# Performance work log

Hardware: AMD Instinct MI355X
Metric: run time of the kernel (lower is better)

Reference implementation:

```python
import jax, jax.numpy as jnp
import numpy as np

HIDDEN = 1024
N_HEADS = 16
HEAD_DIM = HIDDEN // N_HEADS
WINDOW = 256
HALF_W = WINDOW // 2  # 128
GLOBAL_TOKENS = (0,)


def setup_inputs() -> dict:
    key = jax.random.key(0)
    ks = jax.random.split(key, 5)
    B, S = 1, 4096
    scale = 0.02
    return {
        "x": jax.random.normal(ks[0], (B, S, HIDDEN), dtype=jnp.float32),
        "Wq": jax.random.normal(ks[1], (HIDDEN, HIDDEN), dtype=jnp.float32) * scale,
        "Wk": jax.random.normal(ks[2], (HIDDEN, HIDDEN), dtype=jnp.float32) * scale,
        "Wv": jax.random.normal(ks[3], (HIDDEN, HIDDEN), dtype=jnp.float32) * scale,
        "Wo": jax.random.normal(ks[4], (HIDDEN, HIDDEN), dtype=jnp.float32) * scale,
    }


def _longformer_mask(seq_len: int) -> jnp.ndarray:
    # sliding window |i-j| <= half_w, plus full rows/cols for global tokens
    idx = jnp.arange(seq_len)
    mask = jnp.abs(idx[:, None] - idx[None, :]) <= HALF_W
    for g in GLOBAL_TOKENS:
        if 0 <= g < seq_len:
            mask = mask.at[g, :].set(True)
            mask = mask.at[:, g].set(True)
    return mask  # [S, S] bool


def reference(x, Wq, Wk, Wv, Wo):
    B, S, H = x.shape
    scale = HEAD_DIM ** -0.5
    # nn.Linear(bias=False): y = x @ W.T ; split heads -> [B, nH, S, hd]
    def proj(W):
        return jnp.einsum('bsh,oh->bso', x, W).reshape(B, S, N_HEADS, HEAD_DIM).transpose(0, 2, 1, 3)
    q, k, v = proj(Wq), proj(Wk), proj(Wv)
    scores = jnp.einsum('bnsd,bntd->bnst', q, k) * scale  # [B, nH, S, S]
    mask = _longformer_mask(S)
    scores = jnp.where(mask[None, None], scores, jnp.float32(-jnp.inf))
    attn = jax.nn.softmax(scores, axis=-1)
    out = jnp.einsum('bnst,bntd->bnsd', attn, v)  # [B, nH, S, hd]
    out = out.transpose(0, 2, 1, 3).reshape(B, S, H)
    return jnp.einsum('bsh,oh->bso', out, Wo)
```

## Files before the change

kernel.cpp:

```cpp
#include <hip/hip_runtime.h>
#include <hip/hip_bf16.h>
#include <stdint.h>

#define S_LEN 4096
#define HID   1024
#define NH    16
#define HD    64
#define HWIN  128

typedef __bf16 bf16x8 __attribute__((ext_vector_type(8)));
typedef float  f32x4  __attribute__((ext_vector_type(4)));
typedef unsigned short u16x8 __attribute__((ext_vector_type(8)));

typedef const __attribute__((address_space(1))) unsigned int* gas_ptr;
typedef __attribute__((address_space(3))) unsigned int* las_ptr;

__device__ __forceinline__ float bf2f(unsigned short u) {
  union { float f; uint32_t i; } w; w.i = ((uint32_t)u) << 16; return w.f;
}
__device__ __forceinline__ unsigned short f2bf(float f) {
  union { float f; uint32_t i; } w; w.f = f;
  uint32_t r = (w.i + 0x7FFFu + ((w.i >> 16) & 1u)) >> 16;
  return (unsigned short)r;
}

__device__ __forceinline__ void gld_lds16(const void* g, void* l) {
  __builtin_amdgcn_global_load_lds((gas_ptr)g, (las_ptr)l, 16, 0, 0);
}

__global__ __launch_bounds__(256) void convert_all(
    const float* __restrict__ x,
    const float* __restrict__ wq, const float* __restrict__ wk,
    const float* __restrict__ wv, const float* __restrict__ wo,
    unsigned short* __restrict__ xb,
    unsigned short* __restrict__ wqb, unsigned short* __restrict__ wkb,
    unsigned short* __restrict__ wvb, unsigned short* __restrict__ wob) {
  const int XF4 = (S_LEN * HID) / 4;
  const int WF4 = (HID * HID) / 4;
  int i = blockIdx.x * 256 + threadIdx.x;
#pragma unroll
  for (int it = 0; it < 4; it++, i += 524288) {
    const float* in; unsigned short* out; int off;
    if (i < XF4) { in = x; out = xb; off = i; }
    else {
      int j = i - XF4;
      int w = j >> 18;
      off = j & (WF4 - 1);
      switch (w) {
        case 0:  in = wq; out = wqb; break;
        case 1:  in = wk; out = wkb; break;
        case 2:  in = wv; out = wvb; break;
        default: in = wo; out = wob; break;
      }
    }
    float4 v = reinterpret_cast<const float4*>(in)[off];
    ushort4 o;
    o.x = f2bf(v.x); o.y = f2bf(v.y); o.z = f2bf(v.z); o.w = f2bf(v.w);
    reinterpret_cast<ushort4*>(out)[off] = o;
  }
}

__device__ __forceinline__ void gemm_body(const unsigned short* __restrict__ A,
                                          const unsigned short* __restrict__ B,
                                          unsigned short* __restrict__ Cb, int mode) {
  __shared__ __align__(16) unsigned short SM[2 * 128 * 64];
  unsigned short* As = SM;
  unsigned short* Bs = SM + 128 * 64;
  constexpr int K = HID;
  const int tid  = threadIdx.x;
  const int lane = tid & 63;
  const int wave = tid >> 6;
  const int wm = wave >> 1, wn = wave & 1;
  const int m0 = blockIdx.x * 128;
  const int n0 = blockIdx.y * 128;
  const int cl = lane & 15, g = lane >> 4;

  f32x4 acc[4][4];
#pragma unroll
  for (int i = 0; i < 4; i++)
#pragma unroll
    for (int j = 0; j < 4; j++) acc[i][j] = f32x4{0.f, 0.f, 0.f, 0.f};

  const unsigned short* Ap[4];
  const unsigned short* Bp[4];
  int ldso[4];
#pragma unroll
  for (int u = 0; u < 4; u++) {
    int s = tid + u * 256;
    int row = s >> 3, c16 = s & 7;
    int sc = ((c16 ^ (row & 7)) << 3);
    Ap[u] = A + (size_t)(m0 + row) * K + sc;
    Bp[u] = B + (size_t)(n0 + row) * K + sc;
    ldso[u] = s * 8;
  }

  for (int k0 = 0; k0 < K; k0 += 64) {
#pragma unroll
    for (int u = 0; u < 4; u++) {
      gld_lds16(Ap[u] + k0, &As[ldso[u]]);
      gld_lds16(Bp[u] + k0, &Bs[ldso[u]]);
    }
    __syncthreads();
#pragma unroll
    for (int kk = 0; kk < 2; kk++) {
      bf16x8 a[4], b[4];
#pragma unroll
      for (int mi = 0; mi < 4; mi++) {
        int row = wm * 64 + mi * 16 + cl;
        int c16 = (kk * 4 + g) ^ (row & 7);
        a[mi] = *reinterpret_cast<const bf16x8*>(&As[row * 64 + c16 * 8]);
      }
#pragma unroll
      for (int ni = 0; ni < 4; ni++) {
        int row = wn * 64 + ni * 16 + cl;
        int c16 = (kk * 4 + g) ^ (row & 7);
        b[ni] = *reinterpret_cast<const bf16x8*>(&Bs[row * 64 + c16 * 8]);
      }
#pragma unroll
      for (int mi = 0; mi < 4; mi++)
#pragma unroll
        for (int ni = 0; ni < 4; ni++)
          acc[mi][ni] = __builtin_amdgcn_mfma_f32_16x16x32_bf16(a[mi], b[ni], acc[mi][ni], 0, 0, 0);
    }
    __syncthreads();
  }

  const int rl = g * 4;
  if (mode == 1) {
#pragma unroll
    for (int mi = 0; mi < 4; mi++)
#pragma unroll
      for (int ni = 0; ni < 4; ni++) {
        int c = wn * 64 + ni * 16 + cl;
        int slot = (wm * 16 + mi * 4 + g) ^ ((c & 7) << 2);
        uint2 u;
        u.x = (uint32_t)f2bf(acc[mi][ni][0]) | ((uint32_t)f2bf(acc[mi][ni][1]) << 16);
        u.y = (uint32_t)f2bf(acc[mi][ni][2]) | ((uint32_t)f2bf(acc[mi][ni][3]) << 16);
        *reinterpret_cast<uint2*>(&SM[c * 128 + slot * 4]) = u;
      }
    __syncthreads();
    const int rgrp = tid & 15;
#pragma unroll
    for (int p = 0; p < 8; p++) {
      int c = p * 16 + (tid >> 4);
      int sa = (2 * rgrp) ^ ((c & 7) << 2);
      int sb = (2 * rgrp + 1) ^ ((c & 7) << 2);
      uint2 a2 = *reinterpret_cast<const uint2*>(&SM[c * 128 + sa * 4]);
      uint2 b2 = *reinterpret_cast<const uint2*>(&SM[c * 128 + sb * 4]);
      uint4 o{a2.x, a2.y, b2.x, b2.y};
      *reinterpret_cast<uint4*>(&Cb[(size_t)(n0 + c) * S_LEN + m0 + rgrp * 8]) = o;
    }
    return;
  }
#pragma unroll
  for (int mi = 0; mi < 4; mi++)
#pragma unroll
    for (int ni = 0; ni < 4; ni++)
#pragma unroll
      for (int i = 0; i < 4; i++) {
        int r = m0 + wm * 64 + mi * 16 + rl + i;
        int c = n0 + wn * 64 + ni * 16 + cl;
        Cb[(size_t)r * HID + c] = f2bf(acc[mi][ni][i]);
      }
}

__global__ __launch_bounds__(256, 2) void gemm_qkv(
    const unsigned short* __restrict__ xb,
    const unsigned short* __restrict__ wqb, const unsigned short* __restrict__ wkb,
    const unsigned short* __restrict__ wvb,
    unsigned short* __restrict__ Qb, unsigned short* __restrict__ Kb,
    unsigned short* __restrict__ Vt) {
  const unsigned short* B = (blockIdx.z == 0) ? wqb : (blockIdx.z == 1) ? wkb : wvb;
  unsigned short* C       = (blockIdx.z == 0) ? Qb  : (blockIdx.z == 1) ? Kb  : Vt;
  int mode = (blockIdx.z == 2) ? 1 : 0;
  gemm_body(xb, B, C, mode);
}

__global__ __launch_bounds__(256, 2) void gemm_proj(
    unsigned short* __restrict__ Ob, const unsigned short* __restrict__ wob,
    const float* __restrict__ mw, const float* __restrict__ lw,
    const float* __restrict__ ow, float* __restrict__ out) {
  if (blockIdx.x == 0) {
    const float LOG2E = 1.44269504f;
    for (int cc = threadIdx.x; cc < HID; cc += 256) {
      int h = cc >> 6, d = cc & 63;
      float m_g = -1e30f;
#pragma unroll
      for (int c = 0; c < 16; c++) m_g = fmaxf(m_g, mw[h * 16 + c]);
      float lsum = 0.f, osum = 0.f;
#pragma unroll
      for (int c = 0; c < 16; c++) {
        float w = exp2f((mw[h * 16 + c] - m_g) * LOG2E);
        lsum += lw[h * 16 + c] * w;
        osum += ow[(size_t)(h * 16 + c) * HD + d] * w;
      }
      Ob[cc] = f2bf(osum / lsum);
    }
    asm volatile("s_waitcnt vmcnt(0)" ::: "memory");
    __syncthreads();
  }

  __shared__ __align__(16) unsigned short As[128 * 64];
  __shared__ __align__(16) unsigned short Bs[64 * 64];
  constexpr int K = HID;
  const int tid  = threadIdx.x;
  const int lane = tid & 63;
  const int wave = tid >> 6;
  const int wm = wave >> 1, wn = wave & 1;
  const int m0 = blockIdx.x * 128;
  const int n0 = blockIdx.y * 64;
  const int cl = lane & 15, g = lane >> 4;

  f32x4 acc[4][2];
#pragma unroll
  for (int i = 0; i < 4; i++)
#pragma unroll
    for (int j = 0; j < 2; j++) acc[i][j] = f32x4{0.f, 0.f, 0.f, 0.f};

  const unsigned short* Ap[4];
  const unsigned short* Bp[2];
  int ldsoA[4], ldsoB[2];
#pragma unroll
  for (int u = 0; u < 4; u++) {
    int s = tid + u * 256;
    int row = s >> 3, c16 = s & 7;
    Ap[u] = Ob + (size_t)(m0 + row) * K + ((c16 ^ (row & 7)) << 3);
    ldsoA[u] = s * 8;
  }
#pragma unroll
  for (int u = 0; u < 2; u++) {
    int s = tid + u * 256;
    int row = s >> 3, c16 = s & 7;
    Bp[u] = wob + (size_t)(n0 + row) * K + ((c16 ^ (row & 7)) << 3);
    ldsoB[u] = s * 8;
  }

  for (int k0 = 0; k0 < K; k0 += 64) {
#pragma unroll
    for (int u = 0; u < 4; u++) gld_lds16(Ap[u] + k0, &As[ldsoA[u]]);
#pragma unroll
    for (int u = 0; u < 2; u++) gld_lds16(Bp[u] + k0, &Bs[ldsoB[u]]);
    __syncthreads();
#pragma unroll
    for (int kk = 0; kk < 2; kk++) {
      bf16x8 a[4], b[2];
#pragma unroll
      for (int mi = 0; mi < 4; mi++) {
        int row = wm * 64 + mi * 16 + cl;
        int c16 = (kk * 4 + g) ^ (row & 7);
        a[mi] = *reinterpret_cast<const bf16x8*>(&As[row * 64 + c16 * 8]);
      }
#pragma unroll
      for (int ni = 0; ni < 2; ni++) {
        int row = wn * 32 + ni * 16 + cl;
        int c16 = (kk * 4 + g) ^ (row & 7);
        b[ni] = *reinterpret_cast<const bf16x8*>(&Bs[row * 64 + c16 * 8]);
      }
#pragma unroll
      for (int mi = 0; mi < 4; mi++)
#pragma unroll
        for (int ni = 0; ni < 2; ni++)
          acc[mi][ni] = __builtin_amdgcn_mfma_f32_16x16x32_bf16(a[mi], b[ni], acc[mi][ni], 0, 0, 0);
    }
    __syncthreads();
  }

  const int rl = g * 4;
#pragma unroll
  for (int mi = 0; mi < 4; mi++)
#pragma unroll
    for (int ni = 0; ni < 2; ni++)
#pragma unroll
      for (int i = 0; i < 4; i++) {
        int r = m0 + wm * 64 + mi * 16 + rl + i;
        int c = n0 + wn * 32 + ni * 16 + cl;
        out[(size_t)r * HID + c] = acc[mi][ni][i];
      }
}

__global__ __launch_bounds__(256) void attn_win(
    const unsigned short* __restrict__ Qb,
    const unsigned short* __restrict__ Kb,
    const unsigned short* __restrict__ Vt,
    unsigned short* __restrict__ Ob,
    float* __restrict__ mw, float* __restrict__ lw, float* __restrict__ ow) {
  const int tid  = threadIdx.x;
  const int lane = tid & 63;
  const int wave = tid >> 6;

  if (blockIdx.x >= 1024) {
    const int bid = blockIdx.x - 1024;
    const int c = bid & 15, h = bid >> 4;
    const int k = c * 256 + tid;
    __shared__ float qsh[HD];
    __shared__ float ps[256];
    __shared__ float redm[4], redl[4];
    __shared__ float red2[4][HD];
    const float LOG2E = 1.44269504f;

    if (tid < HD) qsh[tid] = bf2f(Qb[h * HD + tid]);
    __syncthreads();

    const unsigned short* kr = Kb + (size_t)k * HID + h * HD;
    float acc = 0.f;
#pragma unroll
    for (int v8 = 0; v8 < 8; v8++) {
      u16x8 kv = *reinterpret_cast<const u16x8*>(kr + v8 * 8);
#pragma unroll
      for (int j = 0; j < 8; j++) acc += qsh[v8 * 8 + j] * bf2f(kv[j]);
    }
    float s = acc * 0.125f;

    float m = s;
#pragma unroll
    for (int d = 1; d < 64; d <<= 1) m = fmaxf(m, __shfl_xor(m, d, 64));
    if (lane == 0) redm[wave] = m;
    __syncthreads();
    float m_c = fmaxf(fmaxf(redm[0], redm[1]), fmaxf(redm[2], redm[3]));

    float p = exp2f((s - m_c) * LOG2E);
    ps[tid] = p;
    float l = p;
#pragma unroll
    for (int d = 1; d < 64; d <<= 1) l += __shfl_xor(l, d, 64);
    if (lane == 0) redl[wave] = l;
    __syncthreads();
    float l_c = redl[0] + redl[1] + redl[2] + redl[3];

    const int d = tid & 63, grp = tid >> 6;
    const unsigned short* vrow = Vt + (size_t)(h * HD + d) * S_LEN + c * 256 + grp * 64;
    float a2 = 0.f;
#pragma unroll
    for (int v8 = 0; v8 < 8; v8++) {
      u16x8 vv = *reinterpret_cast<const u16x8*>(vrow + v8 * 8);
#pragma unroll
      for (int j = 0; j < 8; j++) a2 += ps[grp * 64 + v8 * 8 + j] * bf2f(vv[j]);
    }
    red2[grp][d] = a2;
    __syncthreads();
    if (tid < HD) {
      float o = red2[0][tid] + red2[1][tid] + red2[2][tid] + red2[3][tid];
      ow[(size_t)(h * 16 + c) * HD + tid] = o;
    }
    if (tid == 0) { mw[h * 16 + c] = m_c; lw[h * 16 + c] = l_c; }
    return;
  }

  __shared__ __align__(16) unsigned short Kl[2][64 * 64];
  __shared__ __align__(16) unsigned short Vl[2][64 * 64];
  __shared__ __align__(16) unsigned short Ps[4][16 * 64];
  const int L  = (blockIdx.x & 7) * 128 + (blockIdx.x >> 3);
  const int h  = L >> 6;
  const int q0 = (L & 63) * 64;
  const int qr   = q0 + wave * 16;
  const int cl = lane & 15, g = lane >> 4, rl = g * 4;
  const float SCL = 0.125f * 1.44269504f;

  int kw0 = q0 - 128; if (kw0 < 0) kw0 = 0;
  int kw1 = q0 + 192; if (kw1 > S_LEN) kw1 = S_LEN;
  const int nc = (kw1 - kw0) >> 6;

  const int s0 = tid, s1 = tid + 256;
  const int kr0 = s0 >> 3, kc0 = ((s0 & 7) ^ (kr0 & 7)) << 3;
  const int kr1 = s1 >> 3, kc1 = ((s1 & 7) ^ (kr1 & 7)) << 3;
  const unsigned short* Kbase = Kb + h * HD;
  const unsigned short* Vbase = Vt + (size_t)h * HD * S_LEN;

  auto stage = [&](int kb, int b) {
    gld_lds16(Kbase + (size_t)(kb + kr0) * HID + kc0, &Kl[b][s0 * 8]);
    gld_lds16(Kbase + (size_t)(kb + kr1) * HID + kc1, &Kl[b][s1 * 8]);
    gld_lds16(Vbase + (size_t)kr0 * S_LEN + kb + kc0, &Vl[b][s0 * 8]);
    gld_lds16(Vbase + (size_t)kr1 * S_LEN + kb + kc1, &Vl[b][s1 * 8]);
  };

  stage(kw0, 0);

  bf16x8 qf[2], k0f[2];
  {
    const unsigned short* qb = Qb + (size_t)(qr + cl) * HID + h * HD + g * 8;
    qf[0] = *reinterpret_cast<const bf16x8*>(qb);
    qf[1] = *reinterpret_cast<const bf16x8*>(qb + 32);
    const unsigned short* k0 = Kb + h * HD + g * 8;
    k0f[0] = *reinterpret_cast<const bf16x8*>(k0);
    k0f[1] = *reinterpret_cast<const bf16x8*>(k0 + 32);
  }
  float v0[4];
#pragma unroll
  for (int nt = 0; nt < 4; nt++)
    v0[nt] = bf2f(Vt[(size_t)(h * HD + nt * 16 + cl) * S_LEN]);

  float m_i[4] = {-1e30f, -1e30f, -1e30f, -1e30f};
  float l_i[4] = {0.f, 0.f, 0.f, 0.f};
  f32x4 oacc[4];
#pragma unroll
  for (int nt = 0; nt < 4; nt++) oacc[nt] = f32x4{0.f, 0.f, 0.f, 0.f};

  __syncthreads();

  for (int c = 0; c < nc; c++) {
    const int cur = c & 1;
    const int kb = kw0 + c * 64;
    if (c + 1 < nc) stage(kw0 + (c + 1) * 64, cur ^ 1);

    bf16x8 kf[4][2];
#pragma unroll
    for (int t = 0; t < 4; t++) {
      int R = t * 16 + cl;
      kf[t][0] = *reinterpret_cast<const bf16x8*>(&Kl[cur][R * 64 + ((g ^ (R & 7)) << 3)]);
      kf[t][1] = *reinterpret_cast<const bf16x8*>(&Kl[cur][R * 64 + (((g + 4) ^ (R & 7)) << 3)]);
    }
    f32x4 s4[4];
    __builtin_amdgcn_s_setprio(1);
#pragma unroll
    for (int t = 0; t < 4; t++) {
      s4[t] = f32x4{0.f, 0.f, 0.f, 0.f};
      s4[t] = __builtin_amdgcn_mfma_f32_16x16x32_bf16(qf[0], kf[t][0], s4[t], 0, 0, 0);
      s4[t] = __builtin_amdgcn_mfma_f32_16x16x32_bf16(qf[1], kf[t][1], s4[t], 0, 0, 0);
    }
    __builtin_amdgcn_s_setprio(0);

    float sv[4][4], tm[4];
    if (kb >= qr - 113 && kb <= qr + 65) {
#pragma unroll
      for (int i = 0; i < 4; i++) {
        tm[i] = -1e30f;
#pragma unroll
        for (int t = 0; t < 4; t++) {
          float v = s4[t][i] * SCL;
          sv[t][i] = v;
          tm[i] = fmaxf(tm[i], v);
        }
      }
    } else {
#pragma unroll
      for (int i = 0; i < 4; i++) {
        int row = qr + rl + i;
        tm[i] = -1e30f;
#pragma unroll
        for (int t = 0; t < 4; t++) {
          int col = kb + t * 16 + cl;
          int d = row - col;
          float v = (d <= HWIN && d >= -HWIN) ? s4[t][i] * SCL : -1e30f;
          sv[t][i] = v;
          tm[i] = fmaxf(tm[i], v);
        }
      }
    }

    bool ok = true;
#pragma unroll
    for (int i = 0; i < 4; i++) ok = ok && (tm[i] <= m_i[i] + 8.0f);
    float p[4][4], ps[4];
    if (__all((int)ok)) {
#pragma unroll
      for (int i = 0; i < 4; i++) {
        float sum = 0.f;
#pragma unroll
        for (int t = 0; t < 4; t++) { p[t][i] = exp2f(sv[t][i] - m_i[i]); sum += p[t][i]; }
        ps[i] = sum;
      }
    } else {
#pragma unroll
      for (int dd = 1; dd < 16; dd <<= 1)
#pragma unroll
        for (int i = 0; i < 4; i++) tm[i] = fmaxf(tm[i], __shfl_xor(tm[i], dd, 16));
#pragma unroll
      for (int i = 0; i < 4; i++) {
        float mnew = fmaxf(m_i[i], tm[i]);
        float fac  = exp2f(m_i[i] - mnew);
        m_i[i] = mnew;
        float sum = 0.f;
#pragma unroll
        for (int t = 0; t < 4; t++) { p[t][i] = exp2f(sv[t][i] - mnew); sum += p[t][i]; }
        ps[i] = sum;
        l_i[i] *= fac;
#pragma unroll
        for (int nt = 0; nt < 4; nt++) oacc[nt][i] *= fac;
      }
    }
#pragma unroll
    for (int dd = 1; dd < 16; dd <<= 1)
#pragma unroll
      for (int i = 0; i < 4; i++) ps[i] += __shfl_xor(ps[i], dd, 16);
#pragma unroll
    for (int i = 0; i < 4; i++) l_i[i] += ps[i];

#pragma unroll
    for (int t = 0; t < 4; t++)
#pragma unroll
      for (int i = 0; i < 4; i++) {
        int row = rl + i;
        Ps[wave][row * 64 + ((t * 16 + cl) ^ ((row & 7) << 3))] = f2bf(p[t][i]);
      }
    bf16x8 pf[2];
    pf[0] = *reinterpret_cast<const bf16x8*>(&Ps[wave][cl * 64 + ((g * 8) ^ ((cl & 7) << 3))]);
    pf[1] = *reinterpret_cast<const bf16x8*>(&Ps[wave][cl * 64 + ((32 + g * 8) ^ ((cl & 7) << 3))]);

    __builtin_amdgcn_s_setprio(1);
#pragma unroll
    for (int nt = 0; nt < 4; nt++) {
      int row = nt * 16 + cl;
      bf16x8 vf0 = *reinterpret_cast<const bf16x8*>(&Vl[cur][row * 64 + ((g ^ (row & 7)) << 3)]);
      bf16x8 vf1 = *reinterpret_cast<const bf16x8*>(&Vl[cur][row * 64 + (((g + 4) ^ (row & 7)) << 3)]);
      oacc[nt] = __builtin_amdgcn_mfma_f32_16x16x32_bf16(pf[0], vf0, oacc[nt], 0, 0, 0);
      oacc[nt] = __builtin_amdgcn_mfma_f32_16x16x32_bf16(pf[1], vf1, oacc[nt], 0, 0, 0);
    }
    __builtin_amdgcn_s_setprio(0);

    __syncthreads();
  }

  float part = 0.f;
#pragma unroll
  for (int s = 0; s < 2; s++)
#pragma unroll
    for (int j = 0; j < 8; j++) part += (float)qf[s][j] * (float)k0f[s][j];
  part += __shfl_xor(part, 16);
  part += __shfl_xor(part, 32);
  float s0q = part * SCL;
#pragma unroll
  for (int i = 0; i < 4; i++) {
    float z0 = __shfl(s0q, rl + i, 16);
    int row = qr + rl + i;
    if (row > HWIN) {
      float mnew = fmaxf(m_i[i], z0);
      float fac  = exp2f(m_i[i] - mnew);
      float p0   = exp2f(z0 - mnew);
      l_i[i] = l_i[i] * fac + p0;
#pragma unroll
      for (int nt = 0; nt < 4; nt++)
        oacc[nt][i] = oacc[nt][i] * fac + p0 * v0[nt];
    }
  }

#pragma unroll
  for (int nt = 0; nt < 4; nt++)
#pragma unroll
    for (int i = 0; i < 4; i++)
      Ob[(size_t)(qr + rl + i) * HID + h * HD + nt * 16 + cl] = f2bf(oacc[nt][i] / l_i[i]);
}

extern "C" void kernel_launch(void* const* d_in, const int* in_sizes, int n_in,
                              void* d_out, int out_size, void* d_ws, size_t ws_size,
                              hipStream_t stream) {
  const float* x  = (const float*)d_in[0];
  const float* wq = (const float*)d_in[1];
  const float* wk = (const float*)d_in[2];
  const float* wv = (const float*)d_in[3];
  const float* wo = (const float*)d_in[4];
  float* out = (float*)d_out;
  char* ws = (char*)d_ws;
  const size_t MB = 1024ull * 1024ull;
  unsigned short* xb  = (unsigned short*)(ws + 0 * MB);
  unsigned short* wqb = (unsigned short*)(ws + 8 * MB);
  unsigned short* wkb = (unsigned short*)(ws + 10 * MB);
  unsigned short* wvb = (unsigned short*)(ws + 12 * MB);
  unsigned short* wob = (unsigned short*)(ws + 14 * MB);
  unsigned short* Qb  = (unsigned short*)(ws + 16 * MB);
  unsigned short* Kb  = (unsigned short*)(ws + 24 * MB);
  unsigned short* Vt  = (unsigned short*)(ws + 32 * MB);
  unsigned short* Ob  = (unsigned short*)(ws + 40 * MB);
  float* mw = (float*)(ws + 48 * MB);
  float* lw = (float*)(ws + 48 * MB + 4096);
  float* ow = (float*)(ws + 48 * MB + 8192);

  dim3 blk(256);
  convert_all<<<dim3(2048), blk, 0, stream>>>(
      x, wq, wk, wv, wo, xb, wqb, wkb, wvb, wob);
  gemm_qkv<<<dim3(S_LEN / 128, HID / 128, 3), blk, 0, stream>>>(
      xb, wqb, wkb, wvb, Qb, Kb, Vt);
  attn_win<<<dim3(1280), blk, 0, stream>>>(Qb, Kb, Vt, Ob, mw, lw, ow);
  gemm_proj<<<dim3(S_LEN / 128, HID / 64), blk, 0, stream>>>(
      Ob, wob, mw, lw, ow, out);
}
```

Before: 87.42 us.

## Double attention query tile to 128 rows with 512-thread blocks

The windowed attention kernel now handles 128 query rows per block with 8 waves instead of 64 rows with 4 waves, so each staged K/V chunk is shared by twice as many queries. The key window per block becomes 384 instead of 320 keys, which cuts redundant K/V loads across overlapping windows. Staging uses one 16-byte load per thread for K and V, and the global-token side blocks keep 256 active threads inside a 512-thread block. The trade-off is fewer blocks (512 plus 256), which may reduce occupancy, and half the threads sit idle in the global-token blocks.

```diff
diff --git a/kernel.cpp b/kernel.cpp
--- a/kernel.cpp
+++ b/kernel.cpp
@@ -278,7 +278,7 @@
       }
 }
 
-__global__ __launch_bounds__(256) void attn_win(
+__global__ __launch_bounds__(512) void attn_win(
     const unsigned short* __restrict__ Qb,
     const unsigned short* __restrict__ Kb,
     const unsigned short* __restrict__ Vt,
@@ -288,10 +288,9 @@
   const int lane = tid & 63;
   const int wave = tid >> 6;
 
-  if (blockIdx.x >= 1024) {
-    const int bid = blockIdx.x - 1024;
+  if (blockIdx.x >= 512) {
+    const int bid = blockIdx.x - 512;
     const int c = bid & 15, h = bid >> 4;
-    const int k = c * 256 + tid;
     __shared__ float qsh[HD];
     __shared__ float ps[256];
     __shared__ float redm[4], redl[4];
@@ -301,76 +300,80 @@
     if (tid < HD) qsh[tid] = bf2f(Qb[h * HD + tid]);
     __syncthreads();
 
-    const unsigned short* kr = Kb + (size_t)k * HID + h * HD;
-    float acc = 0.f;
-#pragma unroll
-    for (int v8 = 0; v8 < 8; v8++) {
-      u16x8 kv = *reinterpret_cast<const u16x8*>(kr + v8 * 8);
-#pragma unroll
-      for (int j = 0; j < 8; j++) acc += qsh[v8 * 8 + j] * bf2f(kv[j]);
-    }
-    float s = acc * 0.125f;
-
-    float m = s;
-#pragma unroll
-    for (int d = 1; d < 64; d <<= 1) m = fmaxf(m, __shfl_xor(m, d, 64));
-    if (lane == 0) redm[wave] = m;
+    float sval = 0.f;
+    if (tid < 256) {
+      const int k = c * 256 + tid;
+      const unsigned short* kr = Kb + (size_t)k * HID + h * HD;
+      float acc = 0.f;
+#pragma unroll
+      for (int v8 = 0; v8 < 8; v8++) {
+        u16x8 kv = *reinterpret_cast<const u16x8*>(kr + v8 * 8);
+#pragma unroll
+        for (int j = 0; j < 8; j++) acc += qsh[v8 * 8 + j] * bf2f(kv[j]);
+      }
+      sval = acc * 0.125f;
+      float m = sval;
+#pragma unroll
+      for (int d = 1; d < 64; d <<= 1) m = fmaxf(m, __shfl_xor(m, d, 64));
+      if (lane == 0) redm[wave] = m;
+    }
     __syncthreads();
     float m_c = fmaxf(fmaxf(redm[0], redm[1]), fmaxf(redm[2], redm[3]));
-
-    float p = exp2f((s - m_c) * LOG2E);
-    ps[tid] = p;
-    float l = p;
-#pragma unroll
-    for (int d = 1; d < 64; d <<= 1) l += __shfl_xor(l, d, 64);
-    if (lane == 0) redl[wave] = l;
-    __syncthreads();
-    float l_c = redl[0] + redl[1] + redl[2] + redl[3];
-
-    const int d = tid & 63, grp = tid >> 6;
-    const unsigned short* vrow = Vt + (size_t)(h * HD + d) * S_LEN + c * 256 + grp * 64;
-    float a2 = 0.f;
-#pragma unroll
-    for (int v8 = 0; v8 < 8; v8++) {
-      u16x8 vv = *reinterpret_cast<const u16x8*>(vrow + v8 * 8);
-#pragma unroll
-      for (int j = 0; j < 8; j++) a2 += ps[grp * 64 + v8 * 8 + j] * bf2f(vv[j]);
-    }
-    red2[grp][d] = a2;
+    if (tid < 256) {
+      float p = exp2f((sval - m_c) * LOG2E);
+      ps[tid] = p;
+      float l = p;
+#pragma unroll
+      for (int d = 1; d < 64; d <<= 1) l += __shfl_xor(l, d, 64);
+      if (lane == 0) redl[wave] = l;
+    }
+    __syncthreads();
+    if (tid < 256) {
+      const int d = tid & 63, grp = tid >> 6;
+      const unsigned short* vrow = Vt + (size_t)(h * HD + d) * S_LEN + c * 256 + grp * 64;
+      float a2 = 0.f;
+#pragma unroll
+      for (int v8 = 0; v8 < 8; v8++) {
+        u16x8 vv = *reinterpret_cast<const u16x8*>(vrow + v8 * 8);
+#pragma unroll
+        for (int j = 0; j < 8; j++) a2 += ps[grp * 64 + v8 * 8 + j] * bf2f(vv[j]);
+      }
+      red2[grp][d] = a2;
+    }
     __syncthreads();
     if (tid < HD) {
       float o = red2[0][tid] + red2[1][tid] + red2[2][tid] + red2[3][tid];
       ow[(size_t)(h * 16 + c) * HD + tid] = o;
     }
-    if (tid == 0) { mw[h * 16 + c] = m_c; lw[h * 16 + c] = l_c; }
+    if (tid == 0) {
+      float l_c = redl[0] + redl[1] + redl[2] + redl[3];
+      mw[h * 16 + c] = m_c; lw[h * 16 + c] = l_c;
+    }
     return;
   }
 
   __shared__ __align__(16) unsigned short Kl[2][64 * 64];
   __shared__ __align__(16) unsigned short Vl[2][64 * 64];
-  __shared__ __align__(16) unsigned short Ps[4][16 * 64];
-  const int L  = (blockIdx.x & 7) * 128 + (blockIdx.x >> 3);
-  const int h  = L >> 6;
-  const int q0 = (L & 63) * 64;
+  __shared__ __align__(16) unsigned short Ps[8][16 * 64];
+  const int L  = (blockIdx.x & 7) * 64 + (blockIdx.x >> 3);
+  const int h  = L >> 5;
+  const int q0 = (L & 31) * 128;
   const int qr   = q0 + wave * 16;
   const int cl = lane & 15, g = lane >> 4, rl = g * 4;
   const float SCL = 0.125f * 1.44269504f;
 
   int kw0 = q0 - 128; if (kw0 < 0) kw0 = 0;
-  int kw1 = q0 + 192; if (kw1 > S_LEN) kw1 = S_LEN;
+  int kw1 = q0 + 256; if (kw1 > S_LEN) kw1 = S_LEN;
   const int nc = (kw1 - kw0) >> 6;
 
-  const int s0 = tid, s1 = tid + 256;
-  const int kr0 = s0 >> 3, kc0 = ((s0 & 7) ^ (kr0 & 7)) << 3;
-  const int kr1 = s1 >> 3, kc1 = ((s1 & 7) ^ (kr1 & 7)) << 3;
+  const int sg = tid;
+  const int krow = sg >> 3, kcol = ((sg & 7) ^ (krow & 7)) << 3;
   const unsigned short* Kbase = Kb + h * HD;
   const unsigned short* Vbase = Vt + (size_t)h * HD * S_LEN;
 
   auto stage = [&](int kb, int b) {
-    gld_lds16(Kbase + (size_t)(kb + kr0) * HID + kc0, &Kl[b][s0 * 8]);
-    gld_lds16(Kbase + (size_t)(kb + kr1) * HID + kc1, &Kl[b][s1 * 8]);
-    gld_lds16(Vbase + (size_t)kr0 * S_LEN + kb + kc0, &Vl[b][s0 * 8]);
-    gld_lds16(Vbase + (size_t)kr1 * S_LEN + kb + kc1, &Vl[b][s1 * 8]);
+    gld_lds16(Kbase + (size_t)(kb + krow) * HID + kcol, &Kl[b][sg * 8]);
+    gld_lds16(Vbase + (size_t)krow * S_LEN + kb + kcol, &Vl[b][sg * 8]);
   };
 
   stage(kw0, 0);
@@ -450,14 +453,14 @@
     bool ok = true;
 #pragma unroll
     for (int i = 0; i < 4; i++) ok = ok && (tm[i] <= m_i[i] + 8.0f);
-    float p[4][4], ps[4];
+    float p[4][4], ps2[4];
     if (__all((int)ok)) {
 #pragma unroll
       for (int i = 0; i < 4; i++) {
         float sum = 0.f;
 #pragma unroll
         for (int t = 0; t < 4; t++) { p[t][i] = exp2f(sv[t][i] - m_i[i]); sum += p[t][i]; }
-        ps[i] = sum;
+        ps2[i] = sum;
       }
     } else {
 #pragma unroll
@@ -472,7 +475,7 @@
         float sum = 0.f;
 #pragma unroll
         for (int t = 0; t < 4; t++) { p[t][i] = exp2f(sv[t][i] - mnew); sum += p[t][i]; }
-        ps[i] = sum;
+        ps2[i] = sum;
         l_i[i] *= fac;
 #pragma unroll
         for (int nt = 0; nt < 4; nt++) oacc[nt][i] *= fac;
@@ -481,9 +484,9 @@
 #pragma unroll
     for (int dd = 1; dd < 16; dd <<= 1)
 #pragma unroll
-      for (int i = 0; i < 4; i++) ps[i] += __shfl_xor(ps[i], dd, 16);
-#pragma unroll
-    for (int i = 0; i < 4; i++) l_i[i] += ps[i];
+      for (int i = 0; i < 4; i++) ps2[i] += __shfl_xor(ps2[i], dd, 16);
+#pragma unroll
+    for (int i = 0; i < 4; i++) l_i[i] += ps2[i];
 
 #pragma unroll
     for (int t = 0; t < 4; t++)
@@ -569,7 +572,7 @@
       x, wq, wk, wv, wo, xb, wqb, wkb, wvb, wob);
   gemm_qkv<<<dim3(S_LEN / 128, HID / 128, 3), blk, 0, stream>>>(
       xb, wqb, wkb, wvb, Qb, Kb, Vt);
-  attn_win<<<dim3(1280), blk, 0, stream>>>(Qb, Kb, Vt, Ob, mw, lw, ow);
+  attn_win<<<dim3(768), dim3(512), 0, stream>>>(Qb, Kb, Vt, Ob, mw, lw, ow);
   gemm_proj<<<dim3(S_LEN / 128, HID / 64), blk, 0, stream>>>(
       Ob, wob, mw, lw, ow, out);
 }
```

Result: slower. 92.84 us (+6.2%).
